# Optimization experiments

Measured on AMD Instinct MI355X. Metric: run time of the kernel, lower is better.

## Reference

```python
import jax, jax.numpy as jnp
import numpy as np

N = 4096
IN_F = 512
OUT_F = 256
HEADS = 4
HEAD_DIM = OUT_F // HEADS


def setup_inputs() -> dict:
    key = jax.random.key(0)
    k_feat, k_adj, k_w, k_a = jax.random.split(key, 4)
    features = jax.random.normal(k_feat, (N, IN_F), dtype=jnp.float32)
    adj_matrix = jax.random.uniform(k_adj, (N, N), dtype=jnp.float32)
    # xavier-uniform-ish init scaled small
    W = jax.random.normal(k_w, (OUT_F, IN_F), dtype=jnp.float32) * (1.0 / np.sqrt(IN_F))
    a = jax.random.normal(k_a, (HEADS, 2 * HEAD_DIM), dtype=jnp.float32) * 0.1
    bias = jnp.zeros((OUT_F,), dtype=jnp.float32)
    return {"features": features, "adj_matrix": adj_matrix, "W": W, "a": a, "bias": bias}


def reference(features, adj_matrix, W, a, bias):
    n = features.shape[0]
    h = features @ W.T                      # [N, OUT_F]
    hh = h.reshape(n, HEADS, HEAD_DIM)      # [N, H, D]
    # e[i,j,h] = leaky_relu(<h_i, a[:, :D]> + <h_j, a[:, D:]>) -- additive decomposition
    e_src = jnp.einsum('nhd,hd->nh', hh, a[:, :HEAD_DIM])   # [N, H]
    e_dst = jnp.einsum('nhd,hd->nh', hh, a[:, HEAD_DIM:])   # [N, H]
    e = e_src[:, None, :] + e_dst[None, :, :]               # [N, N, H]
    e = jnp.where(e >= 0, e, 0.2 * e)                       # leaky_relu(0.2)
    mask = adj_matrix[:, :, None] > 0.1                     # [N, N, 1]
    e = jnp.where(mask, e, -jnp.inf)
    attention = jax.nn.softmax(e, axis=1)                   # softmax over j
    attention = jnp.nan_to_num(attention, nan=0.0)          # fully-masked rows -> 0
    attention_mean = attention.mean(axis=2)                 # [N, N]
    h_out = attention_mean @ h + bias                       # [N, OUT_F]
    return h_out
```

## Files before the change

### kernel.cpp

```cpp
#include <hip/hip_runtime.h>
#include <math.h>

#define NN      4096
#define INF_    512
#define OUTF    256
#define NHEAD   4
#define HDIM    64
#define KSPLIT  8

typedef __attribute__((ext_vector_type(8))) short  short8x;
typedef __attribute__((ext_vector_type(4))) float  float4x;
typedef __attribute__((ext_vector_type(2))) float  float2x;

__device__ __forceinline__ unsigned short f2bf(float x) {
    union { float f; unsigned int u; } c; c.f = x;
    unsigned int r = (c.u + 0x7FFFu + ((c.u >> 16) & 1u)) >> 16;
    return (unsigned short)r;
}
__device__ __forceinline__ unsigned int cvtpk_bf16(float lo, float hi) {
    unsigned int r;
    asm("v_cvt_pk_bf16_f32 %0, %1, %2" : "=v"(r) : "v"(lo), "v"(hi));
    return r;
}
__device__ __forceinline__ float2x bf2up(unsigned int u) {
    union { unsigned int x; float f; } lo, hi;
    lo.x = u << 16; hi.x = u & 0xFFFF0000u;
    float2x r; r[0] = lo.f; r[1] = hi.f; return r;
}
__device__ __forceinline__ float2x max2(float2x a, float2x b) {
    float2x r; r[0] = fmaxf(a[0], b[0]); r[1] = fmaxf(a[1], b[1]); return r;
}

__global__ __launch_bounds__(256) void k_hedge(const float* __restrict__ feat,
                                               const float* __restrict__ W,
                                               const float* __restrict__ a,
                                               const float* __restrict__ bias,
                                               const float* __restrict__ adj,
                                               unsigned short* __restrict__ hT,
                                               float* __restrict__ es,
                                               unsigned short* __restrict__ Bt,
                                               unsigned short* __restrict__ Dt,
                                               unsigned short* __restrict__ mask,
                                               float* __restrict__ out) {
    __shared__ __align__(16) unsigned short lds_f[16 * 72];
    __shared__ __align__(16) unsigned short lds_w[256 * 72];
    const int tid  = threadIdx.x;

    if (blockIdx.x >= 256) {
        const int mb = blockIdx.x - 256;
        #pragma unroll
        for (int r = 0; r < 2; ++r) {
            const int row = mb * 2 + r;
            const float4x* arow4 = (const float4x*)(adj + (size_t)row * NN);
            unsigned int bits = 0;
            #pragma unroll
            for (int t = 0; t < 4; ++t) {
                float4x av = arow4[t * 256 + tid];
                #pragma unroll
                for (int e = 0; e < 4; ++e)
                    bits |= (av[e] > 0.1f ? 1u : 0u) << (t * 4 + e);
            }
            mask[(size_t)row * 256 + tid] = (unsigned short)bits;
        }
        return;
    }

    const int w    = tid >> 6;
    const int lane = tid & 63;
    const int lidx = lane & 15;
    const int quad = lane >> 4;
    const int i0   = blockIdx.x * 16;

    {
        float4x bv = *(const float4x*)(bias + ((tid * 4) & 255));
        float* ob = out + (size_t)i0 * OUTF;
        #pragma unroll
        for (int itr = 0; itr < 4; ++itr)
            *(float4x*)(ob + itr * 1024 + tid * 4) = bv;
    }

    const int fr = tid >> 4;
    const int fc = (tid & 15) * 4;
    const int wr = tid >> 2;
    const int wc = (tid & 3) * 16;

    float4x acc[4];
    #pragma unroll
    for (int q = 0; q < 4; ++q)
        acc[q] = (float4x){0.f, 0.f, 0.f, 0.f};

    for (int kt = 0; kt < INF_; kt += 64) {
        __syncthreads();
        {
            float4x v = *(const float4x*)&feat[(size_t)(i0 + fr) * INF_ + kt + fc];
            uint2 u;
            u.x = cvtpk_bf16(v[0], v[1]);
            u.y = cvtpk_bf16(v[2], v[3]);
            *(uint2*)&lds_f[fr * 72 + fc] = u;
        }
        #pragma unroll
        for (int p = 0; p < 4; ++p) {
            int row = p * 64 + wr;
            const float* src = &W[(size_t)row * INF_ + kt + wc];
            float4x v0 = *(const float4x*)(src);
            float4x v1 = *(const float4x*)(src + 4);
            float4x v2 = *(const float4x*)(src + 8);
            float4x v3 = *(const float4x*)(src + 12);
            union { short8x s; unsigned int u[4]; } p0, p1;
            p0.u[0] = cvtpk_bf16(v0[0], v0[1]); p0.u[1] = cvtpk_bf16(v0[2], v0[3]);
            p0.u[2] = cvtpk_bf16(v1[0], v1[1]); p0.u[3] = cvtpk_bf16(v1[2], v1[3]);
            p1.u[0] = cvtpk_bf16(v2[0], v2[1]); p1.u[1] = cvtpk_bf16(v2[2], v2[3]);
            p1.u[2] = cvtpk_bf16(v3[0], v3[1]); p1.u[3] = cvtpk_bf16(v3[2], v3[3]);
            *(short8x*)&lds_w[row * 72 + wc]     = p0.s;
            *(short8x*)&lds_w[row * 72 + wc + 8] = p1.s;
        }
        __syncthreads();
        #pragma unroll
        for (int kk = 0; kk < 2; ++kk) {
            short8x af = *(const short8x*)&lds_f[lidx * 72 + kk * 32 + quad * 8];
            short8x bw[4];
            #pragma unroll
            for (int nt = 0; nt < 4; ++nt)
                bw[nt] = *(const short8x*)&lds_w[(w * 64 + nt * 16 + lidx) * 72 + kk * 32 + quad * 8];
            #pragma unroll
            for (int nt = 0; nt < 4; ++nt)
                acc[nt] = __builtin_amdgcn_mfma_f32_16x16x32_bf16(af, bw[nt], acc[nt], 0, 0, 0);
        }
    }
    #pragma unroll
    for (int nt = 0; nt < 4; ++nt) {
        int col = w * 64 + nt * 16 + lidx;
        uint2 u;
        u.x = cvtpk_bf16(acc[nt][0], acc[nt][1]);
        u.y = cvtpk_bf16(acc[nt][2], acc[nt][3]);
        *(uint2*)&hT[(size_t)col * NN + i0 + quad * 4] = u;
    }
    float asrc[4], adst[4];
    #pragma unroll
    for (int nt = 0; nt < 4; ++nt) {
        asrc[nt] = a[w * 2 * HDIM + nt * 16 + lidx];
        adst[nt] = a[w * 2 * HDIM + HDIM + nt * 16 + lidx];
    }
    #pragma unroll
    for (int r = 0; r < 4; ++r) {
        float s = 0.f, d = 0.f;
        #pragma unroll
        for (int nt = 0; nt < 4; ++nt) {
            s += acc[nt][r] * asrc[nt];
            d += acc[nt][r] * adst[nt];
        }
        #pragma unroll
        for (int off = 1; off < 16; off <<= 1) {
            s += __shfl_xor(s, off);
            d += __shfl_xor(d, off);
        }
        if (lidx == 0) {
            int row = i0 + quad * 4 + r;
            es[row * NHEAD + w] = s;
            Bt[row * NHEAD + w] = f2bf(__expf(d));
            Dt[row * NHEAD + w] = f2bf(__expf(0.2f * d));
        }
    }
}

__global__ __launch_bounds__(256) void k_attn(const unsigned short* __restrict__ mask,
                                              const float* __restrict__ es,
                                              const unsigned short* __restrict__ Bt,
                                              const unsigned short* __restrict__ Dt,
                                              unsigned short* __restrict__ attn) {
    __shared__ float red[4][4];
    __shared__ float cfs[4];
    const int tid = threadIdx.x;
    const int wv  = tid >> 6;
    const int lane = tid & 63;
    const int i = blockIdx.x;

    const float4x esv = ((const float4x*)es)[i];
    float2x A01, A23, C01, C23;
    A01[0] = __expf(esv[0]); A01[1] = __expf(esv[1]);
    A23[0] = __expf(esv[2]); A23[1] = __expf(esv[3]);
    C01[0] = __expf(0.2f * esv[0]); C01[1] = __expf(0.2f * esv[1]);
    C23[0] = __expf(0.2f * esv[2]); C23[1] = __expf(0.2f * esv[3]);

    const unsigned int mbits = mask[(size_t)i * 256 + tid];
    const uint4* B4 = (const uint4*)Bt;
    const uint4* D4 = (const uint4*)Dt;

    float2x m01[4][4], m23[4][4];
    float2x den01 = (float2x){0.f, 0.f};
    float2x den23 = (float2x){0.f, 0.f};
    #pragma unroll
    for (int t = 0; t < 4; ++t) {
        int jv = t * 256 + tid;
        uint4 bu0 = B4[jv * 2], bu1 = B4[jv * 2 + 1];
        uint4 du0 = D4[jv * 2], du1 = D4[jv * 2 + 1];
        unsigned int bwv[8] = {bu0.x, bu0.y, bu0.z, bu0.w, bu1.x, bu1.y, bu1.z, bu1.w};
        unsigned int dwv[8] = {du0.x, du0.y, du0.z, du0.w, du1.x, du1.y, du1.z, du1.w};
        #pragma unroll
        for (int u = 0; u < 4; ++u) {
            float2x b01 = bf2up(bwv[u * 2]);
            float2x b23 = bf2up(bwv[u * 2 + 1]);
            float2x d01 = bf2up(dwv[u * 2]);
            float2x d23 = bf2up(dwv[u * 2 + 1]);
            float mf = (mbits & (1u << (t * 4 + u))) ? 1.f : 0.f;
            float2x mf2; mf2[0] = mf; mf2[1] = mf;
            m01[t][u] = mf2 * max2(A01 * b01, C01 * d01);
            m23[t][u] = mf2 * max2(A23 * b23, C23 * d23);
            den01 += m01[t][u];
            den23 += m23[t][u];
        }
    }
    float dh[4] = {den01[0], den01[1], den23[0], den23[1]};
    #pragma unroll
    for (int off = 1; off < 64; off <<= 1) {
        #pragma unroll
        for (int h = 0; h < 4; ++h)
            dh[h] += __shfl_xor(dh[h], off);
    }
    if (lane == 0) {
        #pragma unroll
        for (int h = 0; h < 4; ++h) red[wv][h] = dh[h];
    }
    __syncthreads();
    if (tid < 4)
        cfs[tid] = red[0][tid] + red[1][tid] + red[2][tid] + red[3][tid];
    __syncthreads();
    float sc[4];
    #pragma unroll
    for (int h = 0; h < 4; ++h) {
        float den = cfs[h];
        sc[h] = den > 0.f ? 0.25f / den : 0.f;
    }

    unsigned short* orow = attn + (size_t)i * NN;
    #pragma unroll
    for (int t = 0; t < 4; ++t) {
        int jv = t * 256 + tid;
        float pv[4];
        #pragma unroll
        for (int u = 0; u < 4; ++u) {
            pv[u] = sc[0] * m01[t][u][0] + sc[1] * m01[t][u][1]
                  + sc[2] * m23[t][u][0] + sc[3] * m23[t][u][1];
        }
        uint2 o;
        o.x = cvtpk_bf16(pv[0], pv[1]);
        o.y = cvtpk_bf16(pv[2], pv[3]);
        *(uint2*)&orow[jv * 4] = o;
    }
}

__global__ __launch_bounds__(256) void k_out_gemm(const unsigned short* __restrict__ attn,
                                                  const unsigned short* __restrict__ hT,
                                                  float* __restrict__ out) {
    __shared__ __align__(16) unsigned short lds_a[32 * 72];
    __shared__ __align__(16) unsigned short lds_h[256 * 72];
    const int tid  = threadIdx.x;
    const int w    = tid >> 6;
    const int lane = tid & 63;
    const int lidx = lane & 15;
    const int quad = lane >> 4;
    const int i0    = blockIdx.x * 32;
    const int kbase = blockIdx.y * (NN / KSPLIT);
    const int sr   = tid >> 3;
    const int sc   = (tid & 7) * 8;

    float4x acc[2][4];
    #pragma unroll
    for (int p = 0; p < 2; ++p)
        #pragma unroll
        for (int q = 0; q < 4; ++q)
            acc[p][q] = (float4x){0.f, 0.f, 0.f, 0.f};

    short8x pa;
    short8x ph[8];
    pa = *(const short8x*)&attn[(size_t)(i0 + sr) * NN + kbase + sc];
    #pragma unroll
    for (int p = 0; p < 8; ++p)
        ph[p] = *(const short8x*)&hT[(size_t)(p * 32 + sr) * NN + kbase + sc];

    const int KSTEPS = (NN / KSPLIT) / 64;
    for (int ks = 0; ks < KSTEPS; ++ks) {
        __syncthreads();
        *(short8x*)&lds_a[sr * 72 + sc] = pa;
        #pragma unroll
        for (int p = 0; p < 8; ++p)
            *(short8x*)&lds_h[(p * 32 + sr) * 72 + sc] = ph[p];
        __syncthreads();
        if (ks + 1 < KSTEPS) {
            const int ko = kbase + (ks + 1) * 64;
            pa = *(const short8x*)&attn[(size_t)(i0 + sr) * NN + ko + sc];
            #pragma unroll
            for (int p = 0; p < 8; ++p)
                ph[p] = *(const short8x*)&hT[(size_t)(p * 32 + sr) * NN + ko + sc];
        }
        #pragma unroll
        for (int kk = 0; kk < 2; ++kk) {
            short8x af[2], bfr[4];
            #pragma unroll
            for (int it = 0; it < 2; ++it)
                af[it]  = *(const short8x*)&lds_a[(it * 16 + lidx) * 72 + kk * 32 + quad * 8];
            #pragma unroll
            for (int nt = 0; nt < 4; ++nt)
                bfr[nt] = *(const short8x*)&lds_h[(w * 64 + nt * 16 + lidx) * 72 + kk * 32 + quad * 8];
            #pragma unroll
            for (int it = 0; it < 2; ++it)
                #pragma unroll
                for (int nt = 0; nt < 4; ++nt)
                    acc[it][nt] = __builtin_amdgcn_mfma_f32_16x16x32_bf16(
                        af[it], bfr[nt], acc[it][nt], 0, 0, 0);
        }
    }
    #pragma unroll
    for (int it = 0; it < 2; ++it)
        #pragma unroll
        for (int nt = 0; nt < 4; ++nt)
            #pragma unroll
            for (int rr = 0; rr < 4; ++rr) {
                int row = i0 + it * 16 + quad * 4 + rr;
                int col = w * 64 + nt * 16 + lidx;
                unsafeAtomicAdd(&out[(size_t)row * OUTF + col], acc[it][nt][rr]);
            }
}

extern "C" void kernel_launch(void* const* d_in, const int* in_sizes, int n_in,
                              void* d_out, int out_size, void* d_ws, size_t ws_size,
                              hipStream_t stream) {
    const float* feat = (const float*)d_in[0];
    const float* adj  = (const float*)d_in[1];
    const float* W    = (const float*)d_in[2];
    const float* a    = (const float*)d_in[3];
    const float* bias = (const float*)d_in[4];
    float* out = (float*)d_out;

    char* ws = (char*)d_ws;
    float*          es    = (float*)(ws + 0);
    unsigned short* Btb   = (unsigned short*)(ws + (64u << 10));
    unsigned short* Dtb   = (unsigned short*)(ws + (96u << 10));
    unsigned short* mask  = (unsigned short*)(ws + (128u << 10));
    unsigned short* hT    = (unsigned short*)(ws + (2560u << 10));
    unsigned short* attn  = (unsigned short*)(ws + (5120u << 10));

    k_hedge    <<<2304,              256, 0, stream>>>(feat, W, a, bias, adj, hT, es, Btb, Dtb, mask, out);
    k_attn     <<<NN,                256, 0, stream>>>(mask, es, Btb, Dtb, attn);
    k_out_gemm <<<dim3(128, KSPLIT), 256, 0, stream>>>(attn, hT, out);
}
```

Baseline: 169.8 us.

## Store h in MFMA fragment layout and load B operands directly from global

The projection kernel now writes h in a pre-swizzled layout that matches the MFMA B-fragment order, so each lane's 8 bf16 values sit contiguously. The output GEMM drops its LDS staging of h and its register prefetch, and reads B fragments straight from global memory with one coalesced 16-byte load per lane. This removes LDS traffic and shrinks LDS use, which may raise occupancy. The cost is that B loads are no longer prefetched a step ahead, so global or L2 latency now sits directly in front of the MFMAs.

Result: no change. 168.8 us (-0.6%).

```diff
diff --git a/kernel.cpp b/kernel.cpp
--- a/kernel.cpp
+++ b/kernel.cpp
@@ -36,7 +36,7 @@
                                                const float* __restrict__ a,
                                                const float* __restrict__ bias,
                                                const float* __restrict__ adj,
-                                               unsigned short* __restrict__ hT,
+                                               unsigned short* __restrict__ hTf,
                                                float* __restrict__ es,
                                                unsigned short* __restrict__ Bt,
                                                unsigned short* __restrict__ Dt,
@@ -127,13 +127,19 @@
                 acc[nt] = __builtin_amdgcn_mfma_f32_16x16x32_bf16(af, bw[nt], acc[nt], 0, 0, 0);
         }
     }
-    #pragma unroll
-    for (int nt = 0; nt < 4; ++nt) {
-        int col = w * 64 + nt * 16 + lidx;
-        uint2 u;
-        u.x = cvtpk_bf16(acc[nt][0], acc[nt][1]);
-        u.y = cvtpk_bf16(acc[nt][2], acc[nt][3]);
-        *(uint2*)&hT[(size_t)col * NN + i0 + quad * 4] = u;
+    {
+        const int ib    = i0 + quad * 4;
+        const int kb2   = ib >> 5;
+        const int quadB = (ib >> 3) & 3;
+        const int e     = ib & 7;
+        #pragma unroll
+        for (int nt = 0; nt < 4; ++nt) {
+            int n16 = w * 4 + nt;
+            uint2 u;
+            u.x = cvtpk_bf16(acc[nt][0], acc[nt][1]);
+            u.y = cvtpk_bf16(acc[nt][2], acc[nt][3]);
+            *(uint2*)&hTf[((size_t)(n16 * 128 + kb2) * 64 + quadB * 16 + lidx) * 8 + e] = u;
+        }
     }
     float asrc[4], adst[4];
     #pragma unroll
@@ -250,10 +256,9 @@
 }
 
 __global__ __launch_bounds__(256) void k_out_gemm(const unsigned short* __restrict__ attn,
-                                                  const unsigned short* __restrict__ hT,
+                                                  const unsigned short* __restrict__ hTf,
                                                   float* __restrict__ out) {
     __shared__ __align__(16) unsigned short lds_a[32 * 72];
-    __shared__ __align__(16) unsigned short lds_h[256 * 72];
     const int tid  = threadIdx.x;
     const int w    = tid >> 6;
     const int lane = tid & 63;
@@ -261,6 +266,7 @@
     const int quad = lane >> 4;
     const int i0    = blockIdx.x * 32;
     const int kbase = blockIdx.y * (NN / KSPLIT);
+    const int kbb   = kbase >> 5;
     const int sr   = tid >> 3;
     const int sc   = (tid & 7) * 8;
 
@@ -272,36 +278,25 @@
             acc[p][q] = (float4x){0.f, 0.f, 0.f, 0.f};
 
     short8x pa;
-    short8x ph[8];
     pa = *(const short8x*)&attn[(size_t)(i0 + sr) * NN + kbase + sc];
-    #pragma unroll
-    for (int p = 0; p < 8; ++p)
-        ph[p] = *(const short8x*)&hT[(size_t)(p * 32 + sr) * NN + kbase + sc];
 
     const int KSTEPS = (NN / KSPLIT) / 64;
     for (int ks = 0; ks < KSTEPS; ++ks) {
         __syncthreads();
         *(short8x*)&lds_a[sr * 72 + sc] = pa;
-        #pragma unroll
-        for (int p = 0; p < 8; ++p)
-            *(short8x*)&lds_h[(p * 32 + sr) * 72 + sc] = ph[p];
         __syncthreads();
-        if (ks + 1 < KSTEPS) {
-            const int ko = kbase + (ks + 1) * 64;
-            pa = *(const short8x*)&attn[(size_t)(i0 + sr) * NN + ko + sc];
-            #pragma unroll
-            for (int p = 0; p < 8; ++p)
-                ph[p] = *(const short8x*)&hT[(size_t)(p * 32 + sr) * NN + ko + sc];
-        }
+        if (ks + 1 < KSTEPS)
+            pa = *(const short8x*)&attn[(size_t)(i0 + sr) * NN + kbase + (ks + 1) * 64 + sc];
         #pragma unroll
         for (int kk = 0; kk < 2; ++kk) {
+            const int kb2 = kbb + ks * 2 + kk;
             short8x af[2], bfr[4];
             #pragma unroll
             for (int it = 0; it < 2; ++it)
                 af[it]  = *(const short8x*)&lds_a[(it * 16 + lidx) * 72 + kk * 32 + quad * 8];
             #pragma unroll
             for (int nt = 0; nt < 4; ++nt)
-                bfr[nt] = *(const short8x*)&lds_h[(w * 64 + nt * 16 + lidx) * 72 + kk * 32 + quad * 8];
+                bfr[nt] = *(const short8x*)&hTf[((size_t)((w * 4 + nt) * 128 + kb2) * 64 + lane) * 8];
             #pragma unroll
             for (int it = 0; it < 2; ++it)
                 #pragma unroll
@@ -337,10 +332,10 @@
     unsigned short* Btb   = (unsigned short*)(ws + (64u << 10));
     unsigned short* Dtb   = (unsigned short*)(ws + (96u << 10));
     unsigned short* mask  = (unsigned short*)(ws + (128u << 10));
-    unsigned short* hT    = (unsigned short*)(ws + (2560u << 10));
+    unsigned short* hTf   = (unsigned short*)(ws + (2560u << 10));
     unsigned short* attn  = (unsigned short*)(ws + (5120u << 10));
 
-    k_hedge    <<<2304,              256, 0, stream>>>(feat, W, a, bias, adj, hT, es, Btb, Dtb, mask, out);
+    k_hedge    <<<2304,              256, 0, stream>>>(feat, W, a, bias, adj, hTf, es, Btb, Dtb, mask, out);
     k_attn     <<<NN,                256, 0, stream>>>(mask, es, Btb, Dtb, attn);
-    k_out_gemm <<<dim3(128, KSPLIT), 256, 0, stream>>>(attn, hT, out);
-}
+    k_out_gemm <<<dim3(128, KSPLIT), 256, 0, stream>>>(attn, hTf, out);
+}
```
